# Kernel optimization log

Hardware: AMD Instinct MI355X
Metric: run time of the kernel (lower is better)

The kernel has to match this reference:

```python
import jax, jax.numpy as jnp
import numpy as np

N_NODES = 50000
N_EDGES = 600000
CHANNELS = 128
HEADS = 8


def setup_inputs() -> dict:
    key = jax.random.key(0)
    k1, k2, k3 = jax.random.split(key, 3)
    x = jax.random.normal(k1, (N_NODES, CHANNELS), dtype=jnp.float32)
    edge_index = jax.random.randint(k2, (2, N_EDGES), 0, N_NODES, dtype=jnp.int32)
    att = jax.random.normal(k3, (HEADS, 2 * (CHANNELS // HEADS)), dtype=jnp.float32)
    return {"x": x, "edge_index": edge_index, "att": att}


def reference(x, edge_index, att):
    # x: [N, C], edge_index: [2, E], att: [H, 2*D] with D = C // H
    src, dst = edge_index[0], edge_index[1]
    n = x.shape[0]
    h = att.shape[0]
    d = att.shape[1] // 2

    x_src = x[src].reshape(-1, h, d)   # [E, H, D]
    x_dst = x[dst].reshape(-1, h, d)   # [E, H, D]

    # (cat([x_src, x_dst]) * att).sum(-1) == x_src @ att[:, :D] + x_dst @ att[:, D:]
    a_src, a_dst = att[:, :d], att[:, d:]
    alpha = jnp.einsum('ehd,hd->eh', x_src, a_src) + jnp.einsum('ehd,hd->eh', x_dst, a_dst)
    alpha = jnp.where(alpha >= 0, alpha, 0.2 * alpha)  # LeakyReLU(0.2)

    # segment softmax over dst; torch scatter_reduce amax includes the zero init,
    # so the per-node max is max(segment_max, 0)
    seg_max = jax.ops.segment_max(alpha, dst, num_segments=n)  # [N, H]
    seg_max = jnp.maximum(seg_max, 0.0)
    alpha = jnp.exp(alpha - seg_max[dst])
    seg_sum = jax.ops.segment_sum(alpha, dst, num_segments=n)  # [N, H]
    alpha = alpha / jnp.maximum(seg_sum[dst], 1e-10)

    # weighted scatter-add of source features
    weighted = x_src * alpha[..., None]                        # [E, H, D]
    out = jax.ops.segment_sum(weighted, dst, num_segments=n)   # [N, H, D]
    return out.reshape(n, -1)
```

## Files before the change

### kernel.cpp

```cpp
#include <hip/hip_runtime.h>

#define N_NODES  50000
#define N_EDGES  600000
#define CHANNELS 128
#define HEADS    8
#define HEAD_DIM 16
#define CAP      64
#define CSTRIDE  4

#define PREP_BLOCK 256
#define EPT        4
#define SCAT_TH    (N_EDGES / EPT)
#define SCAT_VB    ((SCAT_TH + PREP_BLOCK - 1) / PREP_BLOCK)
#define LOGIT_VB   ((N_NODES * (CHANNELS / 4)) / PREP_BLOCK)
#define WPB        4

__global__ void prep_kernel(const float* __restrict__ x,
                            const float* __restrict__ att,
                            const int*   __restrict__ src,
                            const int*   __restrict__ dst,
                            int*            __restrict__ cursor,
                            unsigned short* __restrict__ bucket,
                            float*          __restrict__ ls8,
                            float*          __restrict__ ld8,
                            unsigned short* __restrict__ xb) {
    int b = blockIdx.x;
    if (b < SCAT_VB) {
        int t = b * PREP_BLOCK + threadIdx.x;
        if (t < SCAT_TH) {
#pragma unroll
            for (int k = 0; k < EPT; ++k) {
                int e = t + k * SCAT_TH;
                int d = dst[e];
                int pos = atomicAdd(&cursor[d * CSTRIDE], 1);
                if (pos < CAP) bucket[(size_t)d * CAP + pos] = (unsigned short)src[e];
            }
        }
    } else {
        int gid = (b - SCAT_VB) * PREP_BLOCK + threadIdx.x;
        int n  = gid >> 5;
        int c4 = gid & 31;
        int h  = c4 >> 2;
        int j4 = c4 & 3;

        float4 v = ((const float4*)x)[gid];

        unsigned int ux = __float_as_uint(v.x), uy = __float_as_uint(v.y);
        unsigned int uz = __float_as_uint(v.z), uw = __float_as_uint(v.w);
        ushort4 pk;
        pk.x = (unsigned short)((ux + 0x7FFFu + ((ux >> 16) & 1u)) >> 16);
        pk.y = (unsigned short)((uy + 0x7FFFu + ((uy >> 16) & 1u)) >> 16);
        pk.z = (unsigned short)((uz + 0x7FFFu + ((uz >> 16) & 1u)) >> 16);
        pk.w = (unsigned short)((uw + 0x7FFFu + ((uw >> 16) & 1u)) >> 16);
        ((ushort4*)xb)[gid] = pk;

        float4 as4 = ((const float4*)att)[h * 8 + j4];
        float4 ad4 = ((const float4*)att)[h * 8 + 4 + j4];
        float ts = v.x * as4.x + v.y * as4.y + v.z * as4.z + v.w * as4.w;
        float td = v.x * ad4.x + v.y * ad4.y + v.z * ad4.z + v.w * ad4.w;
        ts += __shfl_xor(ts, 1, 4); ts += __shfl_xor(ts, 2, 4);
        td += __shfl_xor(td, 1, 4); td += __shfl_xor(td, 2, 4);
        if (j4 == 0) {
            ls8[n * HEADS + h] = ts;
            ld8[n * HEADS + h] = td;
        }
    }
}

__global__ void fused_gat_kernel(const unsigned short* __restrict__ xb,
                                 const float* __restrict__ ls8,
                                 const float* __restrict__ ld8,
                                 const int*   __restrict__ cursor,
                                 const unsigned short* __restrict__ bucket,
                                 float*       __restrict__ out) {
    __shared__ float s_p[WPB * CAP * HEADS];

    int wave = threadIdx.x >> 6;
    int lane = threadIdx.x & 63;
    int n = blockIdx.x * WPB + wave;
    if (n >= N_NODES) return;
    int h = lane >> 3;
    int j = lane & 7;

    int   cnt_raw = cursor[n * CSTRIDE];
    int   myidx   = (int)bucket[(size_t)n * CAP + lane];
    float ldst    = ld8[n * HEADS + h];
    int cnt = (cnt_raw > CAP) ? CAP : cnt_raw;

    float* sp = s_p + wave * (CAP * HEADS);

    float av[8];
    float mymax = -1e30f;
#pragma unroll
    for (int k = 0; k < 8; ++k) {
        int i = j + 8 * k;
        av[k] = -1e30f;
        if (i < cnt) {
            int   s  = __shfl(myidx, i);
            float lg = ls8[s * HEADS + h] + ldst;
            float a  = (lg >= 0.0f) ? lg : 0.2f * lg;
            av[k] = a;
            mymax = fmaxf(mymax, a);
        }
    }
#pragma unroll
    for (int o = 4; o >= 1; o >>= 1) mymax = fmaxf(mymax, __shfl_xor(mymax, o, 8));
    float m = fmaxf(mymax, 0.0f);

    float myl = 0.0f;
#pragma unroll
    for (int k = 0; k < 8; ++k) {
        int i = j + 8 * k;
        if (i < cnt) {
            float p = __expf(av[k] - m);
            sp[i * HEADS + h] = p;
            myl += p;
        }
    }
#pragma unroll
    for (int o = 4; o >= 1; o >>= 1) myl += __shfl_xor(myl, o, 8);

#define LQ(k) (((k) < cnt) ? ((const unsigned int*)(xb + (size_t)__shfl(myidx,(k)) * CHANNELS))[lane] : 0u)
    unsigned int q0 = LQ(0), q1 = LQ(1), q2 = LQ(2), q3 = LQ(3);
    unsigned int q4 = LQ(4), q5 = LQ(5), q6 = LQ(6), q7 = LQ(7);

    float ax0 = 0.f, ay0 = 0.f, ax1 = 0.f, ay1 = 0.f;
    int i = 0;
    for (; i + 4 <= cnt; i += 4) {
        float p0 = sp[(i + 0) * HEADS + h];
        float p1 = sp[(i + 1) * HEADS + h];
        float p2 = sp[(i + 2) * HEADS + h];
        float p3 = sp[(i + 3) * HEADS + h];
        ax0 += p0 * __uint_as_float(q0 << 16);
        ay0 += p0 * __uint_as_float(q0 & 0xFFFF0000u);
        ax1 += p1 * __uint_as_float(q1 << 16);
        ay1 += p1 * __uint_as_float(q1 & 0xFFFF0000u);
        ax0 += p2 * __uint_as_float(q2 << 16);
        ay0 += p2 * __uint_as_float(q2 & 0xFFFF0000u);
        ax1 += p3 * __uint_as_float(q3 << 16);
        ay1 += p3 * __uint_as_float(q3 & 0xFFFF0000u);
        q0 = q4; q1 = q5; q2 = q6; q3 = q7;
        q4 = LQ(i + 8); q5 = LQ(i + 9); q6 = LQ(i + 10); q7 = LQ(i + 11);
    }
    for (; i < cnt; ++i) {
        float p = sp[i * HEADS + h];
        ax0 += p * __uint_as_float(q0 << 16);
        ay0 += p * __uint_as_float(q0 & 0xFFFF0000u);
        q0 = q1; q1 = q2; q2 = q3;
    }
#undef LQ

    float inv = 1.0f / fmaxf(myl, 1e-10f);
    *(float2*)(out + (size_t)n * CHANNELS + 2 * lane) =
        make_float2((ax0 + ax1) * inv, (ay0 + ay1) * inv);
}

extern "C" void kernel_launch(void* const* d_in, const int* in_sizes, int n_in,
                              void* d_out, int out_size, void* d_ws, size_t ws_size,
                              hipStream_t stream) {
    const float* x   = (const float*)d_in[0];
    const int*   ei  = (const int*)  d_in[1];
    const float* att = (const float*)d_in[2];
    const int* src = ei;
    const int* dst = ei + N_EDGES;
    float* out = (float*)d_out;

    int*            cursor = (int*)d_ws;
    unsigned short* bucket = (unsigned short*)(cursor + (size_t)N_NODES * CSTRIDE);
    float*          ls8    = (float*)(bucket + (size_t)N_NODES * CAP);
    float*          ld8    = ls8 + (size_t)N_NODES * HEADS;
    unsigned short* xb     = (unsigned short*)(ld8 + (size_t)N_NODES * HEADS);

    hipMemsetAsync(cursor, 0, sizeof(int) * (size_t)N_NODES * CSTRIDE, stream);

    prep_kernel<<<SCAT_VB + LOGIT_VB, PREP_BLOCK, 0, stream>>>(
        x, att, src, dst, cursor, bucket, ls8, ld8, xb);

    {
        int grid = (N_NODES + WPB - 1) / WPB;
        fused_gat_kernel<<<grid, 64 * WPB, 0, stream>>>(
            xb, ls8, ld8, cursor, bucket, out);
    }
}
```

Before: 146.0 us.

## Split wave into two half-waves each gathering 8-byte rows per edge pair

The aggregation loop now has each half of the wave handle alternate edges. Each lane loads a uint2 (four bf16 values) per edge and the two halves are combined with a cross-half shuffle before a float4 store by 32 lanes. This doubles the number of edges in flight per load instruction and widens the loads. The scatter phase batches loads, atomics and stores across 8 edges per thread to overlap atomic latency, and the cursor stride grows to 16 ints to reduce atomic contention on shared cache lines. The cost is a larger cursor memset and more registers for the prefetch buffer.

New measurement: 147.2 us. Within noise of the previous version (+0.9%).

```diff
diff --git a/kernel.cpp b/kernel.cpp
--- a/kernel.cpp
+++ b/kernel.cpp
@@ -6,10 +6,10 @@
 #define HEADS    8
 #define HEAD_DIM 16
 #define CAP      64
-#define CSTRIDE  4
+#define CSTRIDE  16
 
 #define PREP_BLOCK 256
-#define EPT        4
+#define EPT        8
 #define SCAT_TH    (N_EDGES / EPT)
 #define SCAT_VB    ((SCAT_TH + PREP_BLOCK - 1) / PREP_BLOCK)
 #define LOGIT_VB   ((N_NODES * (CHANNELS / 4)) / PREP_BLOCK)
@@ -28,13 +28,20 @@
     if (b < SCAT_VB) {
         int t = b * PREP_BLOCK + threadIdx.x;
         if (t < SCAT_TH) {
+            int dd[EPT], ss[EPT], pp[EPT];
 #pragma unroll
             for (int k = 0; k < EPT; ++k) {
                 int e = t + k * SCAT_TH;
-                int d = dst[e];
-                int pos = atomicAdd(&cursor[d * CSTRIDE], 1);
-                if (pos < CAP) bucket[(size_t)d * CAP + pos] = (unsigned short)src[e];
+                dd[k] = dst[e];
+                ss[k] = src[e];
             }
+#pragma unroll
+            for (int k = 0; k < EPT; ++k)
+                pp[k] = atomicAdd(&cursor[dd[k] * CSTRIDE], 1);
+#pragma unroll
+            for (int k = 0; k < EPT; ++k)
+                if (pp[k] < CAP)
+                    bucket[(size_t)dd[k] * CAP + pp[k]] = (unsigned short)ss[k];
         }
     } else {
         int gid = (b - SCAT_VB) * PREP_BLOCK + threadIdx.x;
@@ -81,6 +88,9 @@
     if (n >= N_NODES) return;
     int h = lane >> 3;
     int j = lane & 7;
+    int r   = lane >> 5;
+    int l32 = lane & 31;
+    int h2  = l32 >> 2;
 
     int   cnt_raw = cursor[n * CSTRIDE];
     int   myidx   = (int)bucket[(size_t)n * CAP + lane];
@@ -120,39 +130,55 @@
 #pragma unroll
     for (int o = 4; o >= 1; o >>= 1) myl += __shfl_xor(myl, o, 8);
 
-#define LQ(k) (((k) < cnt) ? ((const unsigned int*)(xb + (size_t)__shfl(myidx,(k)) * CHANNELS))[lane] : 0u)
-    unsigned int q0 = LQ(0), q1 = LQ(1), q2 = LQ(2), q3 = LQ(3);
-    unsigned int q4 = LQ(4), q5 = LQ(5), q6 = LQ(6), q7 = LQ(7);
-
-    float ax0 = 0.f, ay0 = 0.f, ax1 = 0.f, ay1 = 0.f;
-    int i = 0;
-    for (; i + 4 <= cnt; i += 4) {
-        float p0 = sp[(i + 0) * HEADS + h];
-        float p1 = sp[(i + 1) * HEADS + h];
-        float p2 = sp[(i + 2) * HEADS + h];
-        float p3 = sp[(i + 3) * HEADS + h];
-        ax0 += p0 * __uint_as_float(q0 << 16);
-        ay0 += p0 * __uint_as_float(q0 & 0xFFFF0000u);
-        ax1 += p1 * __uint_as_float(q1 << 16);
-        ay1 += p1 * __uint_as_float(q1 & 0xFFFF0000u);
-        ax0 += p2 * __uint_as_float(q2 << 16);
-        ay0 += p2 * __uint_as_float(q2 & 0xFFFF0000u);
-        ax1 += p3 * __uint_as_float(q3 << 16);
-        ay1 += p3 * __uint_as_float(q3 & 0xFFFF0000u);
-        q0 = q4; q1 = q5; q2 = q6; q3 = q7;
-        q4 = LQ(i + 8); q5 = LQ(i + 9); q6 = LQ(i + 10); q7 = LQ(i + 11);
-    }
-    for (; i < cnt; ++i) {
-        float p = sp[i * HEADS + h];
-        ax0 += p * __uint_as_float(q0 << 16);
-        ay0 += p * __uint_as_float(q0 & 0xFFFF0000u);
-        q0 = q1; q1 = q2; q2 = q3;
-    }
-#undef LQ
-
-    float inv = 1.0f / fmaxf(myl, 1e-10f);
-    *(float2*)(out + (size_t)n * CHANNELS + 2 * lane) =
-        make_float2((ax0 + ax1) * inv, (ay0 + ay1) * inv);
+#define LP(k) ( ((const uint2*)(xb + (size_t)__shfl(myidx, ((2*(k)+r) < cnt) ? (2*(k)+r) : 0) * CHANNELS))[l32] )
+    uint2 q[8];
+#pragma unroll
+    for (int k = 0; k < 8; ++k) q[k] = LP(k);
+
+    float a0 = 0.f, a1 = 0.f, a2 = 0.f, a3 = 0.f;
+    int npair = (cnt + 1) >> 1;
+    int k = 0;
+    for (; k + 4 <= npair; k += 4) {
+#pragma unroll
+        for (int u = 0; u < 4; ++u) {
+            int e2 = 2 * (k + u) + r;
+            float p = (e2 < cnt) ? sp[e2 * HEADS + h2] : 0.0f;
+            uint2 qq = q[u];
+            a0 += p * __uint_as_float(qq.x << 16);
+            a1 += p * __uint_as_float(qq.x & 0xFFFF0000u);
+            a2 += p * __uint_as_float(qq.y << 16);
+            a3 += p * __uint_as_float(qq.y & 0xFFFF0000u);
+        }
+#pragma unroll
+        for (int u = 0; u < 4; ++u) q[u] = q[u + 4];
+#pragma unroll
+        for (int u = 0; u < 4; ++u) q[u + 4] = LP(k + 8 + u);
+    }
+    for (; k < npair; ++k) {
+        int e2 = 2 * k + r;
+        float p = (e2 < cnt) ? sp[e2 * HEADS + h2] : 0.0f;
+        uint2 qq = q[0];
+        a0 += p * __uint_as_float(qq.x << 16);
+        a1 += p * __uint_as_float(qq.x & 0xFFFF0000u);
+        a2 += p * __uint_as_float(qq.y << 16);
+        a3 += p * __uint_as_float(qq.y & 0xFFFF0000u);
+#pragma unroll
+        for (int u = 0; u < 7; ++u) q[u] = q[u + 1];
+    }
+#undef LP
+
+    a0 += __shfl_xor(a0, 32);
+    a1 += __shfl_xor(a1, 32);
+    a2 += __shfl_xor(a2, 32);
+    a3 += __shfl_xor(a3, 32);
+
+    float denom = __shfl(myl, h2 * 8);
+    float inv = 1.0f / fmaxf(denom, 1e-10f);
+
+    if (lane < 32) {
+        float4 o4 = make_float4(a0 * inv, a1 * inv, a2 * inv, a3 * inv);
+        ((float4*)(out + (size_t)n * CHANNELS))[l32] = o4;
+    }
 }
 
 extern "C" void kernel_launch(void* const* d_in, const int* in_sizes, int n_in,
```
